# Kernel tuning notes

Hardware: AMD Instinct MI355X
Metric: run time of the kernel (lower is better)

## Reference

```python
import jax, jax.numpy as jnp
import numpy as np

B, S, E = 2, 2048, 1024
D_ATTN, H = 1024, 16
HD = D_ATTN // H
SCALE = 1.0 / np.sqrt(D_ATTN)
ROPE_BASE = 10000.0


def setup_inputs() -> dict:
    key = jax.random.key(0)
    ks = jax.random.split(key, 7)
    def w(k, shape, scale):
        return jax.random.normal(k, shape, dtype=jnp.float32) * scale
    return {
        "q": w(ks[0], (B, S, E), 1.0),
        "k": w(ks[1], (B, S, E), 1.0),
        "v": w(ks[2], (B, S, E), 1.0),
        "Wq": w(ks[3], (D_ATTN, E), E ** -0.5),
        "Wk": w(ks[4], (D_ATTN, E), E ** -0.5),
        "Wv": w(ks[5], (D_ATTN, E), E ** -0.5),
        "Wo": w(ks[6], (E, D_ATTN), D_ATTN ** -0.5),
    }


def _rope(x):
    # x: [B, H, S, HD]; interleaved-pair rotary embedding over the seq axis
    s, d = x.shape[2], x.shape[3]
    half = d // 2
    inv_freq = 1.0 / (ROPE_BASE ** (jnp.arange(half, dtype=jnp.float32) * 2.0 / d))
    ang = jnp.arange(s, dtype=jnp.float32)[:, None] * inv_freq[None, :]  # [S, half]
    cos, sin = jnp.cos(ang), jnp.sin(ang)
    xr = x.reshape(x.shape[:-1] + (half, 2))
    x0, x1 = xr[..., 0], xr[..., 1]
    o0 = x0 * cos - x1 * sin
    o1 = x0 * sin + x1 * cos
    return jnp.stack([o0, o1], axis=-1).reshape(x.shape)


def reference(q, k, v, Wq, Wk, Wv, Wo):
    # linear projections (nn.Linear with weight [out, in]): y = x @ W^T
    qh = (q @ Wq.T).reshape(B, S, H, HD).transpose(0, 2, 1, 3)  # [B,H,S,HD]
    kh = (k @ Wk.T).reshape(B, S, H, HD).transpose(0, 2, 1, 3)
    vh = (v @ Wv.T).reshape(B, S, H, HD).transpose(0, 2, 1, 3)
    qh = _rope(qh)
    kh = _rope(kh)
    # shifted-causal mask: disallow j >= i (diagonal masked), except (0,0) allowed
    i = jnp.arange(S)[:, None]
    j = jnp.arange(S)[None, :]
    masked = j >= i                              # triu incl. diagonal
    masked = masked.at[0, 0].set(False)          # keep (0,0) so row 0 isn't all -inf
    scores = jnp.einsum("bhsd,bhtd->bhst", qh, kh) * SCALE
    scores = jnp.where(masked, -jnp.inf, scores)
    probs = jax.nn.softmax(scores, axis=-1)      # dropout omitted (eval mode)
    ctx = jnp.einsum("bhst,bhtd->bhsd", probs, vh)
    ctx = ctx.transpose(0, 2, 1, 3).reshape(B, S, D_ATTN)
    return ctx @ Wo.T
```

## Files before the change

### kernel.cpp

```cpp
#include <hip/hip_runtime.h>
#include <hip/hip_bf16.h>

#define BATCH 2
#define SEQ   2048
#define EMB   1024
#define DATTN 1024
#define NH    16
#define HD    64
#define MM    (BATCH*SEQ)
#define SCALE 0.03125f
#define MINIT -1.0e30f
#define ROPE_COEF 0.41524101186f

using bf16x8 = __attribute__((ext_vector_type(8))) short;
using f32x4  = __attribute__((ext_vector_type(4))) float;

__device__ inline short f2bf(float x) {
    __hip_bfloat16 b = __float2bfloat16(x);
    return *reinterpret_cast<short*>(&b);
}

__device__ inline void gl_lds16(const short* g, short* l) {
    __builtin_amdgcn_global_load_lds(
        (const __attribute__((address_space(1))) unsigned int*)g,
        (__attribute__((address_space(3))) unsigned int*)l, 16, 0, 0);
}

__global__ __launch_bounds__(256)
void cvt_all(const float* __restrict__ q, const float* __restrict__ k,
             const float* __restrict__ v,
             const float* __restrict__ Wq, const float* __restrict__ Wk,
             const float* __restrict__ Wv, const float* __restrict__ Wo,
             short* __restrict__ dst)
{
    const long QKV = (long)MM * EMB;
    const long WSZ = (long)DATTN * EMB;
    const long i = ((long)blockIdx.x * 256 + threadIdx.x) * 4;
    const float* s;
    long off;
    if (i < 3 * QKV) {
        const int seg = (int)(i / QKV);
        off = i - (long)seg * QKV;
        s = (seg == 0) ? q : (seg == 1) ? k : v;
    } else {
        const long j = i - 3 * QKV;
        const int seg = (int)(j / WSZ);
        off = j - (long)seg * WSZ;
        s = (seg == 0) ? Wq : (seg == 1) ? Wk : (seg == 2) ? Wv : Wo;
    }
    float4 x = *(const float4*)(s + off);
    short4 y;
    y.x = f2bf(x.x); y.y = f2bf(x.y); y.z = f2bf(x.z); y.w = f2bf(x.w);
    *(short4*)(dst + i) = y;
}

__device__ inline void stage_tile(const short* g, short* lds, int wave, int lane) {
    #pragma unroll
    for (int qq = 0; qq < 2; ++qq) {
        const int r = wave * 32 + qq * 16 + (lane >> 2);
        gl_lds16(g + (long)r * EMB + (lane & 3) * 8, lds + (wave * 2 + qq) * 512);
    }
}

__global__ __launch_bounds__(256)
void gemm_proj_bf16(const short* __restrict__ qb, const short* __restrict__ kb,
                    const short* __restrict__ vb,
                    const short* __restrict__ wqb, const short* __restrict__ wkb,
                    const short* __restrict__ wvb,
                    short* __restrict__ Qb, short* __restrict__ Kb,
                    short* __restrict__ Vtb)
{
    const short* A; const short* B;
    if (blockIdx.z == 0)      { A = qb; B = wqb; }
    else if (blockIdx.z == 1) { A = kb; B = wkb; }
    else                      { A = vb; B = wvb; }

    __shared__ short sA[128 * 32];
    __shared__ short sB[128 * 32];

    const int tid  = threadIdx.x;
    const int wave = tid >> 6, lane = tid & 63;
    const int quad = lane >> 4, l16 = lane & 15;
    const int wm = (wave >> 1) * 64, wn = (wave & 1) * 64;
    const long m0 = (long)blockIdx.x * 128, n0 = (long)blockIdx.y * 128;

    f32x4 acc[4][4];
    #pragma unroll
    for (int i = 0; i < 4; ++i)
        #pragma unroll
        for (int j = 0; j < 4; ++j) acc[i][j] = (f32x4){0.f, 0.f, 0.f, 0.f};

    for (int kt = 0; kt < EMB; kt += 32) {
        __syncthreads();
        stage_tile(A + m0 * EMB + kt, sA, wave, lane);
        stage_tile(B + n0 * EMB + kt, sB, wave, lane);
        __syncthreads();

        bf16x8 af[4], bfr[4];
        #pragma unroll
        for (int rt = 0; rt < 4; ++rt)
            af[rt] = *(const bf16x8*)&sA[(wm + rt * 16 + l16) * 32 + quad * 8];
        #pragma unroll
        for (int ct = 0; ct < 4; ++ct)
            bfr[ct] = *(const bf16x8*)&sB[(wn + ct * 16 + l16) * 32 + quad * 8];
        #pragma unroll
        for (int rt = 0; rt < 4; ++rt)
            #pragma unroll
            for (int ct = 0; ct < 4; ++ct)
                acc[rt][ct] = __builtin_amdgcn_mfma_f32_16x16x32_bf16(
                    af[rt], bfr[ct], acc[rt][ct], 0, 0, 0);
    }

    if (blockIdx.z < 2) {
        short* C = (blockIdx.z == 0) ? Qb : Kb;
        const float scl = (blockIdx.z == 0) ? SCALE : 1.0f;
        const int odd = l16 & 1;
        #pragma unroll
        for (int ct = 0; ct < 4; ++ct) {
            const long col = n0 + wn + ct * 16 + l16;
            const int hh = (int)(col >> 6), dd = (int)(col & (HD - 1));
            const float invf = exp2f(-ROPE_COEF * (float)(dd >> 1));
            #pragma unroll
            for (int rt = 0; rt < 4; ++rt) {
                #pragma unroll
                for (int reg = 0; reg < 4; ++reg) {
                    const long row = m0 + wm + rt * 16 + quad * 4 + reg;
                    const int bb = (int)(row >> 11), ss = (int)(row & (SEQ - 1));
                    const float val = acc[rt][ct][reg];
                    const float prt = __shfl_xor(val, 1, 64);
                    float sn, cs;
                    __sincosf((float)ss * invf, &sn, &cs);
                    const float o = odd ? (prt * sn + val * cs)
                                        : (val * cs - prt * sn);
                    C[(((long)(bb * NH + hh)) << 17) + ((long)ss << 6) + dd] =
                        f2bf(o * scl);
                }
            }
        }
    } else {
        #pragma unroll
        for (int rt = 0; rt < 4; ++rt) {
            #pragma unroll
            for (int ct = 0; ct < 4; ++ct) {
                const long row0 = m0 + wm + rt * 16 + quad * 4;
                const long col  = n0 + wn + ct * 16 + l16;
                const int bb = (int)(row0 >> 11), ss = (int)(row0 & (SEQ - 1));
                const int hh = (int)(col >> 6),   dd = (int)(col & (HD - 1));
                short4 s4;
                s4.x = f2bf(acc[rt][ct][0]); s4.y = f2bf(acc[rt][ct][1]);
                s4.z = f2bf(acc[rt][ct][2]); s4.w = f2bf(acc[rt][ct][3]);
                *(short4*)&Vtb[(((long)(bb * NH + hh)) << 17) + ((long)dd << 11) + ss] = s4;
            }
        }
    }
}

__global__ __launch_bounds__(256)
void gemm_out_bf16(const short* __restrict__ Ab, const short* __restrict__ Bb,
                   float* __restrict__ C)
{
    __shared__ short sA[128 * 32];
    __shared__ short sB[128 * 32];

    const int tid  = threadIdx.x;
    const int wave = tid >> 6, lane = tid & 63;
    const int quad = lane >> 4, l16 = lane & 15;
    const int wm = (wave >> 1) * 64, wn = (wave & 1) * 64;
    const long m0 = (long)blockIdx.x * 128, n0 = (long)blockIdx.y * 128;

    f32x4 acc[4][4];
    #pragma unroll
    for (int i = 0; i < 4; ++i)
        #pragma unroll
        for (int j = 0; j < 4; ++j) acc[i][j] = (f32x4){0.f, 0.f, 0.f, 0.f};

    for (int kt = 0; kt < DATTN; kt += 32) {
        __syncthreads();
        stage_tile(Ab + m0 * DATTN + kt, sA, wave, lane);
        stage_tile(Bb + n0 * DATTN + kt, sB, wave, lane);
        __syncthreads();

        bf16x8 af[4], bfr[4];
        #pragma unroll
        for (int rt = 0; rt < 4; ++rt)
            af[rt] = *(const bf16x8*)&sA[(wm + rt * 16 + l16) * 32 + quad * 8];
        #pragma unroll
        for (int ct = 0; ct < 4; ++ct)
            bfr[ct] = *(const bf16x8*)&sB[(wn + ct * 16 + l16) * 32 + quad * 8];
        #pragma unroll
        for (int rt = 0; rt < 4; ++rt)
            #pragma unroll
            for (int ct = 0; ct < 4; ++ct)
                acc[rt][ct] = __builtin_amdgcn_mfma_f32_16x16x32_bf16(
                    af[rt], bfr[ct], acc[rt][ct], 0, 0, 0);
    }

    #pragma unroll
    for (int rt = 0; rt < 4; ++rt) {
        #pragma unroll
        for (int ct = 0; ct < 4; ++ct) {
            #pragma unroll
            for (int reg = 0; reg < 4; ++reg) {
                const long row = m0 + wm + rt * 16 + quad * 4 + reg;
                const long col = n0 + wn + ct * 16 + l16;
                C[row * EMB + col] = acc[rt][ct][reg];
            }
        }
    }
}

#define LDP 72

__global__ __launch_bounds__(256, 1)
void flash_attn_mfma(const short* __restrict__ Qb,
                     const short* __restrict__ Kb,
                     const short* __restrict__ Vtb,
                     short* __restrict__ ctx)
{
    const int id = blockIdx.x;
    const int r  = id & 7;
    const int q8 = id >> 3;
    const int ts = q8 & 15;
    const int pi = q8 >> 4;
    const int p  = r + 8 * pi;
    const int b  = p >> 4, h = p & 15;
    const int t  = 15 - ts;
    const int tid = threadIdx.x;
    const int wave = tid >> 6, lane = tid & 63;
    const int quad = lane >> 4, l16 = lane & 15;
    const int r0 = t * 128;

    __shared__ short sk2[2][64 * LDP];
    __shared__ short sv2[2][64 * LDP];
    __shared__ short sp[4][16 * LDP];

    const long base = ((long)(b * NH + h)) << 17;

    bf16x8 qf[2][2];
    #pragma unroll
    for (int g = 0; g < 2; ++g)
        #pragma unroll
        for (int tt = 0; tt < 2; ++tt)
            qf[g][tt] = *(const bf16x8*)(Qb + base
                + (long)(r0 + 64 * g + wave * 16 + l16) * HD + tt * 32 + quad * 8);

    f32x4 acc_o[2][4];
    #pragma unroll
    for (int g = 0; g < 2; ++g)
        #pragma unroll
        for (int ct = 0; ct < 4; ++ct) acc_o[g][ct] = (f32x4){0.f, 0.f, 0.f, 0.f};
    float mq[2] = {MINIT, MINIT};
    float lq[2] = {0.f, 0.f};

    const int njt = t + 1;

    #pragma unroll 1
    for (int jt = 0; jt < njt; ++jt) {
        const int jbase = jt * 128;

        __syncthreads();
        #pragma unroll
        for (int c = 0; c < 4; ++c) {
            int cc   = c * 256 + tid;
            int half = cc >> 9;
            int row  = (cc >> 3) & 63;
            int off  = (cc & 7) * 8;
            int4 tK = *(const int4*)(Kb + base
                + (long)(jbase + half * 64 + row) * HD + off);
            *(int4*)&sk2[half][row * LDP + off] = tK;
            int4 tV = *(const int4*)(Vtb + base
                + ((long)row << 11) + jbase + half * 64 + off);
            *(int4*)&sv2[half][row * LDP + off] = tV;
        }
        __syncthreads();

        #pragma unroll
        for (int half = 0; half < 2; ++half) {
            const int jb2 = jbase + half * 64;
            const int jt2 = 2 * jt + half;
            const short* skh = sk2[half];
            const short* svh = sv2[half];

            bf16x8 kf[4][2], vf[4][2];
            #pragma unroll
            for (int ct = 0; ct < 4; ++ct) {
                kf[ct][0] = *(const bf16x8*)&skh[(ct * 16 + l16) * LDP + quad * 8];
                kf[ct][1] = *(const bf16x8*)&skh[(ct * 16 + l16) * LDP + 32 + quad * 8];
                vf[ct][0] = *(const bf16x8*)&svh[(ct * 16 + l16) * LDP + quad * 8];
                vf[ct][1] = *(const bf16x8*)&svh[(ct * 16 + l16) * LDP + 32 + quad * 8];
            }

            short* pw = sp[wave];

            #pragma unroll
            for (int g = 0; g < 2; ++g) {
                if (g == 0 && jt2 == 2 * t + 1) continue;

                f32x4 s[4];
                #pragma unroll
                for (int ct = 0; ct < 4; ++ct) {
                    f32x4 z = (f32x4){0.f, 0.f, 0.f, 0.f};
                    z = __builtin_amdgcn_mfma_f32_16x16x32_bf16(kf[ct][0], qf[g][0], z, 0, 0, 0);
                    z = __builtin_amdgcn_mfma_f32_16x16x32_bf16(kf[ct][1], qf[g][1], z, 0, 0, 0);
                    s[ct] = z;
                }

                const int iq = r0 + 64 * g + wave * 16 + l16;
                if (jt2 == 2 * t + g) {
                    #pragma unroll
                    for (int ct = 0; ct < 4; ++ct)
                        #pragma unroll
                        for (int rr = 0; rr < 4; ++rr) {
                            const int j = jb2 + ct * 16 + quad * 4 + rr;
                            const bool ok = (j < iq) || (iq == 0 && j == 0);
                            if (!ok) s[ct][rr] = -INFINITY;
                        }
                }

                float mx = MINIT;
                #pragma unroll
                for (int ct = 0; ct < 4; ++ct)
                    #pragma unroll
                    for (int rr = 0; rr < 4; ++rr) mx = fmaxf(mx, s[ct][rr]);
                mx = fmaxf(mx, __shfl_xor(mx, 16, 64));
                mx = fmaxf(mx, __shfl_xor(mx, 32, 64));
                const float mn = fmaxf(mq[g], mx);
                const float alpha = __expf(mq[g] - mn);
                mq[g] = mn;
                float ss = 0.f;
                #pragma unroll
                for (int ct = 0; ct < 4; ++ct)
                    #pragma unroll
                    for (int rr = 0; rr < 4; ++rr) {
                        const float e = __expf(s[ct][rr] - mn);
                        s[ct][rr] = e;
                        ss += e;
                    }
                ss += __shfl_xor(ss, 16, 64);
                ss += __shfl_xor(ss, 32, 64);
                lq[g] = lq[g] * alpha + ss;

                #pragma unroll
                for (int ct = 0; ct < 4; ++ct) {
                    short4 p4;
                    p4.x = f2bf(s[ct][0]); p4.y = f2bf(s[ct][1]);
                    p4.z = f2bf(s[ct][2]); p4.w = f2bf(s[ct][3]);
                    *(short4*)&pw[l16 * LDP + ct * 16 + quad * 4] = p4;
                }

                #pragma unroll
                for (int ct = 0; ct < 4; ++ct)
                    #pragma unroll
                    for (int rr = 0; rr < 4; ++rr) acc_o[g][ct][rr] *= alpha;

                bf16x8 pf0 = *(const bf16x8*)&pw[l16 * LDP + quad * 8];
                bf16x8 pf1 = *(const bf16x8*)&pw[l16 * LDP + 32 + quad * 8];
                #pragma unroll
                for (int ct = 0; ct < 4; ++ct) {
                    acc_o[g][ct] = __builtin_amdgcn_mfma_f32_16x16x32_bf16(
                        vf[ct][0], pf0, acc_o[g][ct], 0, 0, 0);
                    acc_o[g][ct] = __builtin_amdgcn_mfma_f32_16x16x32_bf16(
                        vf[ct][1], pf1, acc_o[g][ct], 0, 0, 0);
                }
            }
        }
    }

    #pragma unroll
    for (int g = 0; g < 2; ++g) {
        const float inv = 1.f / lq[g];
        const int iq = r0 + 64 * g + wave * 16 + l16;
        short* orow = ctx + (long)(b * SEQ + iq) * DATTN + h * HD;
        #pragma unroll
        for (int ct = 0; ct < 4; ++ct) {
            short4 o4;
            o4.x = f2bf(acc_o[g][ct][0] * inv);
            o4.y = f2bf(acc_o[g][ct][1] * inv);
            o4.z = f2bf(acc_o[g][ct][2] * inv);
            o4.w = f2bf(acc_o[g][ct][3] * inv);
            *(short4*)&orow[ct * 16 + quad * 4] = o4;
        }
    }
}

extern "C" void kernel_launch(void* const* d_in, const int* in_sizes, int n_in,
                              void* d_out, int out_size, void* d_ws, size_t ws_size,
                              hipStream_t stream) {
    const float* q  = (const float*)d_in[0];
    const float* k  = (const float*)d_in[1];
    const float* v  = (const float*)d_in[2];
    const float* Wq = (const float*)d_in[3];
    const float* Wk = (const float*)d_in[4];
    const float* Wv = (const float*)d_in[5];
    const float* Wo = (const float*)d_in[6];
    float* out = (float*)d_out;

    const long QKV = (long)MM * EMB;
    const long WSZ = (long)DATTN * EMB;
    short* basep = (short*)d_ws;
    short* qb  = basep;
    short* kb  = qb + QKV;
    short* vb  = kb + QKV;
    short* wqb = vb + QKV;
    short* wkb = wqb + WSZ;
    short* wvb = wkb + WSZ;
    short* wob = wvb + WSZ;
    short* Qb  = wob + WSZ;
    short* Kb  = Qb + QKV;
    short* Vtb = Kb + QKV;
    short* ctx = Vtb + QKV;

    cvt_all<<<16384, 256, 0, stream>>>(q, k, v, Wq, Wk, Wv, Wo, qb);

    gemm_proj_bf16<<<dim3(MM / 128, DATTN / 128, 3), 256, 0, stream>>>(
        qb, kb, vb, wqb, wkb, wvb, Qb, Kb, Vtb);

    flash_attn_mfma<<<512, 256, 0, stream>>>(Qb, Kb, Vtb, ctx);

    gemm_out_bf16<<<dim3(MM / 128, EMB / 128), 256, 0, stream>>>(ctx, wob, out);
}
```

Measured before the change: 248.3 us.

## Halve flash-attention query tile to 64 rows and double grid size

Each attention block now handles 64 query rows instead of 128 (one row group per wave instead of two), and the grid grows from 512 to 1024 blocks. K/V tiles are still loaded 128 keys at a time, and the upper half is skipped once it lies past the causal diagonal. The aim is more parallelism and better load balance across CUs on the causal triangle, with fewer registers per thread. The cost is that each K/V tile is reused by half as many queries, so global K/V traffic roughly doubles.

```diff
diff --git a/kernel.cpp b/kernel.cpp
--- a/kernel.cpp
+++ b/kernel.cpp
@@ -220,15 +220,15 @@
     const int id = blockIdx.x;
     const int r  = id & 7;
     const int q8 = id >> 3;
-    const int ts = q8 & 15;
-    const int pi = q8 >> 4;
+    const int ts = q8 & 31;
+    const int pi = q8 >> 5;
     const int p  = r + 8 * pi;
     const int b  = p >> 4, h = p & 15;
-    const int t  = 15 - ts;
+    const int t  = 31 - ts;
     const int tid = threadIdx.x;
     const int wave = tid >> 6, lane = tid & 63;
     const int quad = lane >> 4, l16 = lane & 15;
-    const int r0 = t * 128;
+    const int r0 = t * 64;
 
     __shared__ short sk2[2][64 * LDP];
     __shared__ short sv2[2][64 * LDP];
@@ -236,23 +236,18 @@
 
     const long base = ((long)(b * NH + h)) << 17;
 
-    bf16x8 qf[2][2];
-    #pragma unroll
-    for (int g = 0; g < 2; ++g)
-        #pragma unroll
-        for (int tt = 0; tt < 2; ++tt)
-            qf[g][tt] = *(const bf16x8*)(Qb + base
-                + (long)(r0 + 64 * g + wave * 16 + l16) * HD + tt * 32 + quad * 8);
-
-    f32x4 acc_o[2][4];
-    #pragma unroll
-    for (int g = 0; g < 2; ++g)
-        #pragma unroll
-        for (int ct = 0; ct < 4; ++ct) acc_o[g][ct] = (f32x4){0.f, 0.f, 0.f, 0.f};
-    float mq[2] = {MINIT, MINIT};
-    float lq[2] = {0.f, 0.f};
-
-    const int njt = t + 1;
+    const int iq = r0 + wave * 16 + l16;
+    bf16x8 qf[2];
+    #pragma unroll
+    for (int tt = 0; tt < 2; ++tt)
+        qf[tt] = *(const bf16x8*)(Qb + base + (long)iq * HD + tt * 32 + quad * 8);
+
+    f32x4 acc_o[4];
+    #pragma unroll
+    for (int ct = 0; ct < 4; ++ct) acc_o[ct] = (f32x4){0.f, 0.f, 0.f, 0.f};
+    float mq = MINIT, lq = 0.f;
+
+    const int njt = (t + 2) >> 1;
 
     #pragma unroll 1
     for (int jt = 0; jt < njt; ++jt) {
@@ -276,8 +271,9 @@
 
         #pragma unroll
         for (int half = 0; half < 2; ++half) {
+            const int jt2 = 2 * jt + half;
+            if (jt2 > t) continue;
             const int jb2 = jbase + half * 64;
-            const int jt2 = 2 * jt + half;
             const short* skh = sk2[half];
             const short* svh = sv2[half];
 
@@ -290,96 +286,85 @@
                 vf[ct][1] = *(const bf16x8*)&svh[(ct * 16 + l16) * LDP + 32 + quad * 8];
             }
 
-            short* pw = sp[wave];
-
-            #pragma unroll
-            for (int g = 0; g < 2; ++g) {
-                if (g == 0 && jt2 == 2 * t + 1) continue;
-
-                f32x4 s[4];
-                #pragma unroll
-                for (int ct = 0; ct < 4; ++ct) {
-                    f32x4 z = (f32x4){0.f, 0.f, 0.f, 0.f};
-                    z = __builtin_amdgcn_mfma_f32_16x16x32_bf16(kf[ct][0], qf[g][0], z, 0, 0, 0);
-                    z = __builtin_amdgcn_mfma_f32_16x16x32_bf16(kf[ct][1], qf[g][1], z, 0, 0, 0);
-                    s[ct] = z;
-                }
-
-                const int iq = r0 + 64 * g + wave * 16 + l16;
-                if (jt2 == 2 * t + g) {
-                    #pragma unroll
-                    for (int ct = 0; ct < 4; ++ct)
-                        #pragma unroll
-                        for (int rr = 0; rr < 4; ++rr) {
-                            const int j = jb2 + ct * 16 + quad * 4 + rr;
-                            const bool ok = (j < iq) || (iq == 0 && j == 0);
-                            if (!ok) s[ct][rr] = -INFINITY;
-                        }
-                }
-
-                float mx = MINIT;
-                #pragma unroll
-                for (int ct = 0; ct < 4; ++ct)
-                    #pragma unroll
-                    for (int rr = 0; rr < 4; ++rr) mx = fmaxf(mx, s[ct][rr]);
-                mx = fmaxf(mx, __shfl_xor(mx, 16, 64));
-                mx = fmaxf(mx, __shfl_xor(mx, 32, 64));
-                const float mn = fmaxf(mq[g], mx);
-                const float alpha = __expf(mq[g] - mn);
-                mq[g] = mn;
-                float ss = 0.f;
+            f32x4 s[4];
+            #pragma unroll
+            for (int ct = 0; ct < 4; ++ct) {
+                f32x4 z = (f32x4){0.f, 0.f, 0.f, 0.f};
+                z = __builtin_amdgcn_mfma_f32_16x16x32_bf16(kf[ct][0], qf[0], z, 0, 0, 0);
+                z = __builtin_amdgcn_mfma_f32_16x16x32_bf16(kf[ct][1], qf[1], z, 0, 0, 0);
+                s[ct] = z;
+            }
+
+            if (jt2 == t) {
                 #pragma unroll
                 for (int ct = 0; ct < 4; ++ct)
                     #pragma unroll
                     for (int rr = 0; rr < 4; ++rr) {
-                        const float e = __expf(s[ct][rr] - mn);
-                        s[ct][rr] = e;
-                        ss += e;
+                        const int j = jb2 + ct * 16 + quad * 4 + rr;
+                        const bool ok = (j < iq) || (iq == 0 && j == 0);
+                        if (!ok) s[ct][rr] = -INFINITY;
                     }
-                ss += __shfl_xor(ss, 16, 64);
-                ss += __shfl_xor(ss, 32, 64);
-                lq[g] = lq[g] * alpha + ss;
-
+            }
+
+            float mx = MINIT;
+            #pragma unroll
+            for (int ct = 0; ct < 4; ++ct)
                 #pragma unroll
-                for (int ct = 0; ct < 4; ++ct) {
-                    short4 p4;
-                    p4.x = f2bf(s[ct][0]); p4.y = f2bf(s[ct][1]);
-                    p4.z = f2bf(s[ct][2]); p4.w = f2bf(s[ct][3]);
-                    *(short4*)&pw[l16 * LDP + ct * 16 + quad * 4] = p4;
+                for (int rr = 0; rr < 4; ++rr) mx = fmaxf(mx, s[ct][rr]);
+            mx = fmaxf(mx, __shfl_xor(mx, 16, 64));
+            mx = fmaxf(mx, __shfl_xor(mx, 32, 64));
+            const float mn = fmaxf(mq, mx);
+            const float alpha = __expf(mq - mn);
+            mq = mn;
+            float ss = 0.f;
+            #pragma unroll
+            for (int ct = 0; ct < 4; ++ct)
+                #pragma unroll
+                for (int rr = 0; rr < 4; ++rr) {
+                    const float e = __expf(s[ct][rr] - mn);
+                    s[ct][rr] = e;
+                    ss += e;
                 }
-
+            ss += __shfl_xor(ss, 16, 64);
+            ss += __shfl_xor(ss, 32, 64);
+            lq = lq * alpha + ss;
+
+            short* pw = sp[wave];
+            #pragma unroll
+            for (int ct = 0; ct < 4; ++ct) {
+                short4 p4;
+                p4.x = f2bf(s[ct][0]); p4.y = f2bf(s[ct][1]);
+                p4.z = f2bf(s[ct][2]); p4.w = f2bf(s[ct][3]);
+                *(short4*)&pw[l16 * LDP + ct * 16 + quad * 4] = p4;
+            }
+
+            #pragma unroll
+            for (int ct = 0; ct < 4; ++ct)
                 #pragma unroll
-                for (int ct = 0; ct < 4; ++ct)
-                    #pragma unroll
-                    for (int rr = 0; rr < 4; ++rr) acc_o[g][ct][rr] *= alpha;
-
-                bf16x8 pf0 = *(const bf16x8*)&pw[l16 * LDP + quad * 8];
-                bf16x8 pf1 = *(const bf16x8*)&pw[l16 * LDP + 32 + quad * 8];
-                #pragma unroll
-                for (int ct = 0; ct < 4; ++ct) {
-                    acc_o[g][ct] = __builtin_amdgcn_mfma_f32_16x16x32_bf16(
-                        vf[ct][0], pf0, acc_o[g][ct], 0, 0, 0);
-                    acc_o[g][ct] = __builtin_amdgcn_mfma_f32_16x16x32_bf16(
-                        vf[ct][1], pf1, acc_o[g][ct], 0, 0, 0);
-                }
+                for (int rr = 0; rr < 4; ++rr) acc_o[ct][rr] *= alpha;
+
+            bf16x8 pf0 = *(const bf16x8*)&pw[l16 * LDP + quad * 8];
+            bf16x8 pf1 = *(const bf16x8*)&pw[l16 * LDP + 32 + quad * 8];
+            #pragma unroll
+            for (int ct = 0; ct < 4; ++ct) {
+                acc_o[ct] = __builtin_amdgcn_mfma_f32_16x16x32_bf16(
+                    vf[ct][0], pf0, acc_o[ct], 0, 0, 0);
+                acc_o[ct] = __builtin_amdgcn_mfma_f32_16x16x32_bf16(
+                    vf[ct][1], pf1, acc_o[ct], 0, 0, 0);
             }
         }
     }
 
-    #pragma unroll
-    for (int g = 0; g < 2; ++g) {
-        const float inv = 1.f / lq[g];
-        const int iq = r0 + 64 * g + wave * 16 + l16;
-        short* orow = ctx + (long)(b * SEQ + iq) * DATTN + h * HD;
-        #pragma unroll
-        for (int ct = 0; ct < 4; ++ct) {
-            short4 o4;
-            o4.x = f2bf(acc_o[g][ct][0] * inv);
-            o4.y = f2bf(acc_o[g][ct][1] * inv);
-            o4.z = f2bf(acc_o[g][ct][2] * inv);
-            o4.w = f2bf(acc_o[g][ct][3] * inv);
-            *(short4*)&orow[ct * 16 + quad * 4] = o4;
-        }
+    const float inv = 1.f / lq;
+    short* orow = ctx + (long)(b * SEQ + iq) * DATTN + h * HD;
+    #pragma unroll
+    for (int ct = 0; ct < 4; ++ct) {
+        short4 o4;
+        o4.x = f2bf(acc_o[ct][0] * inv);
+        o4.y = f2bf(acc_o[ct][1] * inv);
+        o4.z = f2bf(acc_o[ct][2] * inv);
+        o4.w = f2bf(acc_o[ct][3] * inv);
+        *(short4*)&orow[ct * 16 + quad * 4] = o4;
     }
 }
 
@@ -415,7 +400,7 @@
     gemm_proj_bf16<<<dim3(MM / 128, DATTN / 128, 3), 256, 0, stream>>>(
         qb, kb, vb, wqb, wkb, wvb, Qb, Kb, Vtb);
 
-    flash_attn_mfma<<<512, 256, 0, stream>>>(Qb, Kb, Vtb, ctx);
+    flash_attn_mfma<<<1024, 256, 0, stream>>>(Qb, Kb, Vtb, ctx);
 
     gemm_out_bf16<<<dim3(MM / 128, EMB / 128), 256, 0, stream>>>(ctx, wob, out);
 }
```

Measured after the change: 236.9 us. -4.6%, faster.
